# Performance work log

Measured on AMD Instinct MI355X. Metric: run time of the kernel, lower is better.

## Reference

```python
import jax, jax.numpy as jnp
import numpy as np
import math

B, N, D = 8, 2048, 64


def setup_inputs() -> dict:
    key = jax.random.key(0)
    kq, kk, kv, kd = jax.random.split(key, 4)
    Q = jax.random.normal(kq, (B, N, D), dtype=jnp.float32)
    K = jax.random.normal(kk, (B, N, D), dtype=jnp.float32)
    V = jax.random.normal(kv, (B, N, D), dtype=jnp.float32)
    dist_matrix = jax.random.uniform(kd, (N, N), dtype=jnp.float32)
    return {"Q": Q, "K": K, "V": V, "dist_matrix": dist_matrix}


def rescale_distance_matrix(dist_matrix):
    # (1 + e^1) / (1 + exp(1 - dist))
    c = 1.0
    return (c + math.e) / (c + jnp.exp(c - dist_matrix))


def reference(Q, K, V, dist_matrix):
    d_k = K.shape[-1]
    inv_sqrt_dk = 1.0 / math.sqrt(d_k)
    # [B, N, N] raw attention logits
    qk = jnp.einsum("bnd,bmd->bnm", Q, K)
    # ReLU then multiply by rescaled distance matrix [N, N] on the right
    scores = jnp.matmul(jax.nn.relu(qk), rescale_distance_matrix(dist_matrix)) * inv_sqrt_dk
    attn = jax.nn.softmax(scores, axis=-1)
    context = jnp.einsum("bnm,bmd->bnd", attn, V)
    return context
```

## Files before the change

kernel.cpp:

```cpp
#include <hip/hip_runtime.h>


typedef _Float16 f16;
typedef _Float16 f16x8 __attribute__((ext_vector_type(8)));
typedef float    f32x4 __attribute__((ext_vector_type(4)));

#define AS1C(p) ((const __attribute__((address_space(1))) void*)(p))
#define AS3(p)  ((__attribute__((address_space(3))) void*)(p))

__device__ __forceinline__ f16x8 cvt_f16x8(float4 a, float4 b){
  f16x8 v;
  v[0]=(f16)a.x; v[1]=(f16)a.y; v[2]=(f16)a.z; v[3]=(f16)a.w;
  v[4]=(f16)b.x; v[5]=(f16)b.y; v[6]=(f16)b.z; v[7]=(f16)b.w;
  return v;
}

__global__ void k_rescaleT(const float* __restrict__ Dm, f16* __restrict__ RhT){
  __shared__ f16 tl[64][65];
  const int k0 = blockIdx.x*64, m0 = blockIdx.y*64;
  const int t = threadIdx.x, c = t & 63, g = t >> 6;
#pragma unroll
  for (int i=0;i<16;++i){
    int k = g*16 + i;
    float d = Dm[(size_t)(k0 + k)*2048 + m0 + c];
    tl[k][c] = (f16)(3.7182818284590452f / (1.0f + __expf(1.0f - d)));
  }
  __syncthreads();
#pragma unroll
  for (int i=0;i<16;++i){
    int m = g*16 + i;
    RhT[(size_t)(m0 + m)*2048 + k0 + c] = tl[c][m];
  }
}

__global__ void k_vT(const float* __restrict__ V, f16* __restrict__ VhT){
  __shared__ f16 tl[64][65];
  const int b = blockIdx.y, m0 = blockIdx.x*64;
  const int t = threadIdx.x, c = t & 63, g = t >> 6;
#pragma unroll
  for (int i=0;i<16;++i){
    int m = g*16 + i;
    tl[m][c] = (f16)V[((size_t)b*2048 + m0 + m)*64 + c];
  }
  __syncthreads();
#pragma unroll
  for (int i=0;i<16;++i){
    int d = g*16 + i;
    VhT[((size_t)b*64 + d)*2048 + m0 + c] = tl[c][d];
  }
}

__launch_bounds__(256, 2)
__global__ void k_qk(const float* __restrict__ Q, const float* __restrict__ Km,
                     f16* __restrict__ Ph){
  __shared__ char shm[36864];
  f16* Qt = (f16*)shm;
  f16* Kt = (f16*)(shm + 18432);
  f16* Tt = (f16*)shm;

  const int t = threadIdx.x, w = t>>6, l = t&63, lr = l&15, q = l>>4;
  const int b = blockIdx.z, n0 = blockIdx.y*128, m0 = blockIdx.x*128;
  const int wr = (w>>1)*64, wc = (w&1)*64;
  const float* Qb = Q  + ((size_t)b*2048 + n0)*64;
  const float* Kb = Km + ((size_t)b*2048 + m0)*64;

  const int sr = t>>3, sc = t&7;
#pragma unroll
  for (int j=0;j<4;++j){
    int row = sr + 32*j;
    const float* p  = Qb + (size_t)row*64 + sc*8;
    *(f16x8*)(Qt + row*72 + sc*8) = cvt_f16x8(*(const float4*)p, *(const float4*)(p+4));
    const float* pk = Kb + (size_t)row*64 + sc*8;
    *(f16x8*)(Kt + row*72 + sc*8) = cvt_f16x8(*(const float4*)pk, *(const float4*)(pk+4));
  }
  __syncthreads();

  f32x4 acc[4][4] = {};
#pragma unroll
  for (int kc=0;kc<2;++kc){
    f16x8 af[4], bf[4];
#pragma unroll
    for (int ti=0;ti<4;++ti) af[ti] = *(const f16x8*)(Qt + (wr+16*ti+lr)*72 + kc*32 + q*8);
#pragma unroll
    for (int tj=0;tj<4;++tj) bf[tj] = *(const f16x8*)(Kt + (wc+16*tj+lr)*72 + kc*32 + q*8);
#pragma unroll
    for (int ti=0;ti<4;++ti)
#pragma unroll
      for (int tj=0;tj<4;++tj)
        acc[ti][tj] = __builtin_amdgcn_mfma_f32_16x16x32_f16(af[ti], bf[tj], acc[ti][tj], 0,0,0);
  }
  __syncthreads();
#pragma unroll
  for (int ti=0;ti<4;++ti)
#pragma unroll
    for (int tj=0;tj<4;++tj)
#pragma unroll
      for (int r=0;r<4;++r)
        Tt[(wr+16*ti+4*q+r)*136 + wc+16*tj+lr] = (f16)(fmaxf(acc[ti][tj][r],0.f)*0.125f);
  __syncthreads();
  const int g16 = t&15, r0 = t>>4;
#pragma unroll
  for (int j=0;j<8;++j){
    int row = r0 + 16*j;
    *(f16x8*)(Ph + ((size_t)b*2048 + n0 + row)*2048 + m0 + g16*8) =
        *(const f16x8*)(Tt + row*136 + g16*8);
  }
}

__launch_bounds__(256, 2)
__global__ void k_attn(const f16* __restrict__ Ph, const f16* __restrict__ RhT,
                       const f16* __restrict__ VhT, f16* __restrict__ Op,
                       float* __restrict__ mp, float* __restrict__ lp){
  __shared__ char smem[54272];
  f16*  Pbuf = (f16*)smem;
  f16*  Rbuf = (f16*)(smem + 16384);
  f16*  El   = (f16*)smem;
  float* stat_max = (float*)(smem + 49152);
  float* stat_sum = (float*)(smem + 51200);
  float* mrow = (float*)(smem + 53248);
  float* lrow = (float*)(smem + 53760);

  const int t = threadIdx.x, w = t>>6, l = t&63, lr = l&15, q = l>>4;
  const int bid = blockIdx.x;
  const int jq = bid & 3, nbb = bid >> 2, b = nbb & 7, nb = nbb >> 3;
  const int n0 = nb*128, jbase = jq*512;
  const int wc = w*64;

  const f16* Pblk = Ph  + ((size_t)b*2048 + n0)*2048;
  const f16* Vb   = VhT + (size_t)b*64*2048;

  if (t < 128){ mrow[t] = -1e30f; lrow[t] = 0.0f; }

  f32x4 Oacc[2][2][2] = {};
  const int swz = (lr>>1)&3;

  auto stage = [&](int jg, int kc){
    const int cb = kc & 1, k0 = kc*32;
#pragma unroll
    for (int i=0;i<2;++i){
      int slot = i*256 + t;
      int row = slot>>2, g = slot&3;
      int gs = (g ^ ((row>>1)&3))*8;
      __builtin_amdgcn_global_load_lds(AS1C(Pblk + (size_t)row*2048 + k0 + gs),
                                       AS3(Pbuf + cb*4096 + i*2048 + w*512), 16, 0, 0);
    }
#pragma unroll
    for (int i=0;i<4;++i){
      int slot = i*256 + t;
      int row = slot>>2, g = slot&3;
      int gs = (g ^ ((row>>1)&3))*8;
      __builtin_amdgcn_global_load_lds(AS1C(RhT + (size_t)(jg + row)*2048 + k0 + gs),
                                       AS3(Rbuf + cb*8192 + i*2048 + w*512), 16, 0, 0);
    }
  };

  stage(jbase, 0);

  for (int mt = 0; mt < 2; ++mt){
    const int jg = jbase + mt*256;
    f32x4 acc[8][4] = {};

#pragma unroll 2
    for (int kc = 0; kc < 64; ++kc){
      __syncthreads();
      if (kc < 63) stage(jg, kc+1);
      const int cb = kc & 1;
      const f16* Pb = Pbuf + cb*4096;
      const f16* Rb = Rbuf + cb*8192;
      f16x8 bf[4];
#pragma unroll
      for (int tj=0;tj<4;++tj)
        bf[tj] = *(const f16x8*)(Rb + (wc + 16*tj + lr)*32 + (q ^ swz)*8);
#pragma unroll
      for (int ti=0;ti<8;++ti){
        f16x8 af = *(const f16x8*)(Pb + (16*ti + lr)*32 + (q ^ swz)*8);
#pragma unroll
        for (int tj=0;tj<4;++tj)
          acc[ti][tj] = __builtin_amdgcn_mfma_f32_16x16x32_f16(af, bf[tj], acc[ti][tj], 0,0,0);
      }
    }

#pragma unroll
    for (int p=0;p<2;++p){
      float pm[4][4];
#pragma unroll
      for (int ti=0;ti<4;++ti)
#pragma unroll
        for (int r=0;r<4;++r)
          pm[ti][r] = fmaxf(fmaxf(acc[4*p+ti][0][r], acc[4*p+ti][1][r]),
                            fmaxf(acc[4*p+ti][2][r], acc[4*p+ti][3][r]));
#pragma unroll
      for (int mm=1;mm<16;mm<<=1)
#pragma unroll
        for (int ti=0;ti<4;++ti)
#pragma unroll
          for (int r=0;r<4;++r)
            pm[ti][r] = fmaxf(pm[ti][r], __shfl_xor(pm[ti][r], mm));
      if (lr == 0)
#pragma unroll
        for (int ti=0;ti<4;++ti)
#pragma unroll
          for (int r=0;r<4;++r)
            stat_max[(64*p + 16*ti + 4*q + r)*4 + w] = pm[ti][r];
      __syncthreads();

      float Mn[4][4], ps[4][4], al[2][4];
#pragma unroll
      for (int ti=0;ti<4;++ti)
#pragma unroll
        for (int r=0;r<4;++r){
          int row = 64*p + 16*ti + 4*q + r;
          float4 s4 = *(const float4*)&stat_max[row*4];
          float tm = fmaxf(fmaxf(s4.x,s4.y), fmaxf(s4.z,s4.w));
          float mo = mrow[row];
          float M  = fmaxf(mo, tm);
          Mn[ti][r] = M;
          ps[ti][r] = 0.f;
          if ((ti>>1) == (w&1)) al[ti&1][r] = __expf(mo - M);
        }
#pragma unroll
      for (int ti=0;ti<4;++ti)
#pragma unroll
        for (int tj=0;tj<4;++tj)
#pragma unroll
          for (int r=0;r<4;++r){
            float e = __expf(acc[4*p+ti][tj][r] - Mn[ti][r]);
            ps[ti][r] += e;
            El[(16*ti + 4*q + r)*264 + wc + 16*tj + lr] = (f16)e;
          }
#pragma unroll
      for (int mm=1;mm<16;mm<<=1)
#pragma unroll
        for (int ti=0;ti<4;++ti)
#pragma unroll
          for (int r=0;r<4;++r)
            ps[ti][r] += __shfl_xor(ps[ti][r], mm);
      if (lr == 0)
#pragma unroll
        for (int ti=0;ti<4;++ti)
#pragma unroll
          for (int r=0;r<4;++r)
            stat_sum[(64*p + 16*ti + 4*q + r)*4 + w] = ps[ti][r];
#pragma unroll
      for (int a=0;a<2;++a)
#pragma unroll
        for (int bb=0;bb<2;++bb)
#pragma unroll
          for (int r=0;r<4;++r)
            Oacc[p][a][bb][r] *= al[a][r];
      __syncthreads();

      if (t < 64){
        int row = 64*p + t;
        float m_o = mrow[row], tm = -1e30f, s4 = 0.f;
#pragma unroll
        for (int i=0;i<4;++i){ tm = fmaxf(tm, stat_max[row*4+i]); s4 += stat_sum[row*4+i]; }
        float M = fmaxf(m_o, tm);
        lrow[row] = lrow[row]*__expf(m_o - M) + s4;
        mrow[row] = M;
      }

      const int erb = 32*(w&1), vcb = 32*(w>>1);
#pragma unroll
      for (int ks=0; ks<8; ++ks){
        f16x8 ae[2], bv[2];
#pragma unroll
        for (int a=0;a<2;++a)
          ae[a] = *(const f16x8*)(El + (erb + 16*a + lr)*264 + ks*32 + q*8);
#pragma unroll
        for (int bb=0;bb<2;++bb)
          bv[bb] = *(const f16x8*)(Vb + (size_t)(vcb + 16*bb + lr)*2048 + jg + ks*32 + q*8);
#pragma unroll
        for (int a=0;a<2;++a)
#pragma unroll
          for (int bb=0;bb<2;++bb)
            Oacc[p][a][bb] = __builtin_amdgcn_mfma_f32_16x16x32_f16(ae[a], bv[bb], Oacc[p][a][bb], 0,0,0);
      }
      __syncthreads();
    }

    if (mt == 0) stage(jbase + 256, 0);
  }

  __syncthreads();
#pragma unroll
  for (int p=0;p<2;++p)
#pragma unroll
    for (int a=0;a<2;++a)
#pragma unroll
      for (int bb=0;bb<2;++bb)
#pragma unroll
        for (int r=0;r<4;++r){
          int row = 64*p + 32*(w&1) + 16*a + 4*q + r;
          int col = 32*(w>>1) + 16*bb + lr;
          Op[((size_t)bid*128 + row)*64 + col] = (f16)Oacc[p][a][bb][r];
        }
  if (t < 128){ mp[bid*128 + t] = mrow[t]; lp[bid*128 + t] = lrow[t]; }
}

__global__ void k_comb(const f16* __restrict__ Op, const float* __restrict__ mp,
                       const float* __restrict__ lp, float* __restrict__ out){
  const int rb = blockIdx.x;
  const int b = rb & 7, nb = rb >> 3;
  const int bid0 = rb*4;
  const int t = threadIdx.x;
  const int row = t >> 1, half = t & 1;

  float m_[4], a_[4];
  float M = -1e30f, den = 0.f;
#pragma unroll
  for (int i=0;i<4;++i){ m_[i] = mp[(bid0+i)*128 + row]; M = fmaxf(M, m_[i]); }
#pragma unroll
  for (int i=0;i<4;++i){ a_[i] = __expf(m_[i] - M); den += a_[i]*lp[(bid0+i)*128 + row]; }
  float inv = 1.0f / den;

#pragma unroll
  for (int g=0;g<4;++g){
    int c0 = half*32 + g*8;
    float o[8] = {};
#pragma unroll
    for (int i=0;i<4;++i){
      f16x8 v = *(const f16x8*)(Op + ((size_t)(bid0+i)*128 + row)*64 + c0);
#pragma unroll
      for (int e=0;e<8;++e) o[e] += a_[i]*(float)v[e];
    }
    float4 o0, o1;
    o0.x=o[0]*inv; o0.y=o[1]*inv; o0.z=o[2]*inv; o0.w=o[3]*inv;
    o1.x=o[4]*inv; o1.y=o[5]*inv; o1.z=o[6]*inv; o1.w=o[7]*inv;
    float* dst = out + ((size_t)b*2048 + nb*128 + row)*64 + c0;
    *(float4*)dst = o0;
    *(float4*)(dst+4) = o1;
  }
}

extern "C" void kernel_launch(void* const* d_in, const int* in_sizes, int n_in,
                              void* d_out, int out_size, void* d_ws, size_t ws_size,
                              hipStream_t stream){
  (void)in_sizes; (void)n_in; (void)out_size; (void)ws_size;
  const float* Q  = (const float*)d_in[0];
  const float* K  = (const float*)d_in[1];
  const float* V  = (const float*)d_in[2];
  const float* Dm = (const float*)d_in[3];
  float* out = (float*)d_out;
  char* ws = (char*)d_ws;
  f16* Ph  = (f16*)ws;
  f16* RhT = (f16*)(ws + (size_t)64*1024*1024);
  f16* VhT = (f16*)(ws + (size_t)72*1024*1024);
  f16* Op  = (f16*)(ws + (size_t)74*1024*1024);
  float* mpp = (float*)(ws + (size_t)74*1024*1024 + (size_t)512*128*64*2);
  float* lpp = mpp + 512*128;

  k_rescaleT<<<dim3(32,32), 256, 0, stream>>>(Dm, RhT);
  k_vT      <<<dim3(32,8),  256, 0, stream>>>(V, VhT);
  k_qk      <<<dim3(16,16,8), 256, 0, stream>>>(Q, K, Ph);
  k_attn    <<<dim3(512),   256, 0, stream>>>(Ph, RhT, VhT, Op, mpp, lpp);
  k_comb    <<<dim3(128),   256, 0, stream>>>(Op, mpp, lpp, out);
}
```

Before: 260.1 us.

## Fuse QK^T+ReLU into attention kernel, recomputing P tiles on the fly

New measurement: 272.3 us. 1.05x slower.

```diff
diff --git a/kernel.cpp b/kernel.cpp
--- a/kernel.cpp
+++ b/kernel.cpp
@@ -50,239 +50,226 @@
   }
 }
 
+__global__ void k_cvtK(const float* __restrict__ K, f16* __restrict__ Kh){
+  size_t i = ((size_t)blockIdx.x*256 + threadIdx.x)*8;
+  *(f16x8*)(Kh + i) = cvt_f16x8(*(const float4*)(K+i), *(const float4*)(K+i+4));
+}
+
 __launch_bounds__(256, 2)
-__global__ void k_qk(const float* __restrict__ Q, const float* __restrict__ Km,
-                     f16* __restrict__ Ph){
-  __shared__ char shm[36864];
-  f16* Qt = (f16*)shm;
-  f16* Kt = (f16*)(shm + 18432);
-  f16* Tt = (f16*)shm;
-
-  const int t = threadIdx.x, w = t>>6, l = t&63, lr = l&15, q = l>>4;
-  const int b = blockIdx.z, n0 = blockIdx.y*128, m0 = blockIdx.x*128;
-  const int wr = (w>>1)*64, wc = (w&1)*64;
-  const float* Qb = Q  + ((size_t)b*2048 + n0)*64;
-  const float* Kb = Km + ((size_t)b*2048 + m0)*64;
-
-  const int sr = t>>3, sc = t&7;
-#pragma unroll
-  for (int j=0;j<4;++j){
-    int row = sr + 32*j;
-    const float* p  = Qb + (size_t)row*64 + sc*8;
-    *(f16x8*)(Qt + row*72 + sc*8) = cvt_f16x8(*(const float4*)p, *(const float4*)(p+4));
-    const float* pk = Kb + (size_t)row*64 + sc*8;
-    *(f16x8*)(Kt + row*72 + sc*8) = cvt_f16x8(*(const float4*)pk, *(const float4*)(pk+4));
-  }
-  __syncthreads();
-
-  f32x4 acc[4][4] = {};
-#pragma unroll
-  for (int kc=0;kc<2;++kc){
-    f16x8 af[4], bf[4];
-#pragma unroll
-    for (int ti=0;ti<4;++ti) af[ti] = *(const f16x8*)(Qt + (wr+16*ti+lr)*72 + kc*32 + q*8);
-#pragma unroll
-    for (int tj=0;tj<4;++tj) bf[tj] = *(const f16x8*)(Kt + (wc+16*tj+lr)*72 + kc*32 + q*8);
-#pragma unroll
-    for (int ti=0;ti<4;++ti)
-#pragma unroll
-      for (int tj=0;tj<4;++tj)
-        acc[ti][tj] = __builtin_amdgcn_mfma_f32_16x16x32_f16(af[ti], bf[tj], acc[ti][tj], 0,0,0);
-  }
-  __syncthreads();
-#pragma unroll
-  for (int ti=0;ti<4;++ti)
-#pragma unroll
-    for (int tj=0;tj<4;++tj)
-#pragma unroll
-      for (int r=0;r<4;++r)
-        Tt[(wr+16*ti+4*q+r)*136 + wc+16*tj+lr] = (f16)(fmaxf(acc[ti][tj][r],0.f)*0.125f);
-  __syncthreads();
-  const int g16 = t&15, r0 = t>>4;
-#pragma unroll
-  for (int j=0;j<8;++j){
-    int row = r0 + 16*j;
-    *(f16x8*)(Ph + ((size_t)b*2048 + n0 + row)*2048 + m0 + g16*8) =
-        *(const f16x8*)(Tt + row*136 + g16*8);
-  }
-}
-
-__launch_bounds__(256, 2)
-__global__ void k_attn(const f16* __restrict__ Ph, const f16* __restrict__ RhT,
-                       const f16* __restrict__ VhT, f16* __restrict__ Op,
-                       float* __restrict__ mp, float* __restrict__ lp){
-  __shared__ char smem[54272];
+__global__ void k_attn(const float* __restrict__ Q, const f16* __restrict__ Kh,
+                       const f16* __restrict__ RhT, const f16* __restrict__ VhT,
+                       f16* __restrict__ Op, float* __restrict__ mp,
+                       float* __restrict__ lp){
+  __shared__ char smem[62464];
   f16*  Pbuf = (f16*)smem;
-  f16*  Rbuf = (f16*)(smem + 16384);
+  f16*  Kbuf = (f16*)(smem + 16384);
+  f16*  Rbuf = (f16*)(smem + 24576);
   f16*  El   = (f16*)smem;
-  float* stat_max = (float*)(smem + 49152);
-  float* stat_sum = (float*)(smem + 51200);
-  float* mrow = (float*)(smem + 53248);
-  float* lrow = (float*)(smem + 53760);
+  float* stat_max = (float*)(smem + 57344);
+  float* stat_sum = (float*)(smem + 59392);
+  float* mrow = (float*)(smem + 61440);
+  float* lrow = (float*)(smem + 61952);
 
   const int t = threadIdx.x, w = t>>6, l = t&63, lr = l&15, q = l>>4;
   const int bid = blockIdx.x;
-  const int jq = bid & 3, nbb = bid >> 2, b = nbb & 7, nb = nbb >> 3;
-  const int n0 = nb*128, jbase = jq*512;
+  const int jq = bid & 7, nbb = bid >> 3, b = nbb & 7, nb = nbb >> 3;
+  const int n0 = nb*128, jg = jq*256;
   const int wc = w*64;
 
-  const f16* Pblk = Ph  + ((size_t)b*2048 + n0)*2048;
-  const f16* Vb   = VhT + (size_t)b*64*2048;
+  const float* Qb = Q   + ((size_t)b*2048 + n0)*64;
+  const f16*  Khb = Kh  + (size_t)b*2048*64;
+  const f16*  Vb  = VhT + (size_t)b*64*2048;
 
   if (t < 128){ mrow[t] = -1e30f; lrow[t] = 0.0f; }
 
+  f16x8 qf[2][2];
+#pragma unroll
+  for (int a=0;a<2;++a)
+#pragma unroll
+    for (int dc=0;dc<2;++dc){
+      const float* p = Qb + (size_t)(32*w + 16*a + lr)*64 + dc*32 + q*8;
+      qf[a][dc] = cvt_f16x8(*(const float4*)p, *(const float4*)(p+4));
+    }
+
   f32x4 Oacc[2][2][2] = {};
-  const int swz = (lr>>1)&3;
-
-  auto stage = [&](int jg, int kc){
+  const int swz  = (lr>>1)&3;
+  const int kswz = lr&7;
+
+  auto stageK = [&](int kc){
+    const int cb = kc & 1;
+    int row = t>>3, g = t&7;
+    int gs = (g ^ (row&7))*8;
+    __builtin_amdgcn_global_load_lds(AS1C(Khb + (size_t)(kc*32 + row)*64 + gs),
+                                     AS3(Kbuf + cb*2048 + w*512), 16, 0, 0);
+  };
+  auto stageR = [&](int kc){
     const int cb = kc & 1, k0 = kc*32;
 #pragma unroll
-    for (int i=0;i<2;++i){
-      int slot = i*256 + t;
-      int row = slot>>2, g = slot&3;
-      int gs = (g ^ ((row>>1)&3))*8;
-      __builtin_amdgcn_global_load_lds(AS1C(Pblk + (size_t)row*2048 + k0 + gs),
-                                       AS3(Pbuf + cb*4096 + i*2048 + w*512), 16, 0, 0);
-    }
-#pragma unroll
     for (int i=0;i<4;++i){
-      int slot = i*256 + t;
-      int row = slot>>2, g = slot&3;
+      int slot = i*256 + t, row = slot>>2, g = slot&3;
       int gs = (g ^ ((row>>1)&3))*8;
       __builtin_amdgcn_global_load_lds(AS1C(RhT + (size_t)(jg + row)*2048 + k0 + gs),
                                        AS3(Rbuf + cb*8192 + i*2048 + w*512), 16, 0, 0);
     }
   };
-
-  stage(jbase, 0);
-
-  for (int mt = 0; mt < 2; ++mt){
-    const int jg = jbase + mt*256;
-    f32x4 acc[8][4] = {};
-
+  auto computeP = [&](int kc){
+    const int cb = kc & 1;
+    const f16* Kb = Kbuf + cb*2048;
+    f16x8 bf[2][2];
+#pragma unroll
+    for (int bb=0;bb<2;++bb)
+#pragma unroll
+      for (int dc=0;dc<2;++dc)
+        bf[bb][dc] = *(const f16x8*)(Kb + (16*bb + lr)*64 + ((dc*4 + q) ^ kswz)*8);
+    f32x4 pa[2][2] = {};
+#pragma unroll
+    for (int dc=0;dc<2;++dc)
+#pragma unroll
+      for (int a=0;a<2;++a)
+#pragma unroll
+        for (int bb=0;bb<2;++bb)
+          pa[a][bb] = __builtin_amdgcn_mfma_f32_16x16x32_f16(qf[a][dc], bf[bb][dc], pa[a][bb], 0,0,0);
+    f16* Pw = Pbuf + cb*4096;
+#pragma unroll
+    for (int a=0;a<2;++a)
+#pragma unroll
+      for (int bb=0;bb<2;++bb)
+#pragma unroll
+        for (int r=0;r<4;++r){
+          int row = 32*w + 16*a + 4*q + r;
+          int m   = 16*bb + lr;
+          Pw[row*32 + ((m>>3) ^ ((row>>1)&3))*8 + (m&7)] =
+              (f16)(fmaxf(pa[a][bb][r], 0.f)*0.125f);
+        }
+  };
+
+  stageK(0);
+  __syncthreads();
+  stageR(0); stageK(1);
+  computeP(0);
+
+  f32x4 acc[8][4] = {};
 #pragma unroll 2
-    for (int kc = 0; kc < 64; ++kc){
-      __syncthreads();
-      if (kc < 63) stage(jg, kc+1);
-      const int cb = kc & 1;
-      const f16* Pb = Pbuf + cb*4096;
-      const f16* Rb = Rbuf + cb*8192;
-      f16x8 bf[4];
+  for (int kc = 0; kc < 64; ++kc){
+    __syncthreads();
+    if (kc < 63) stageR(kc+1);
+    if (kc < 62) stageK(kc+2);
+    if (kc < 63) computeP(kc+1);
+    const int cb = kc & 1;
+    const f16* Pb = Pbuf + cb*4096;
+    const f16* Rb = Rbuf + cb*8192;
+    f16x8 bf2[4];
+#pragma unroll
+    for (int tj=0;tj<4;++tj)
+      bf2[tj] = *(const f16x8*)(Rb + (wc + 16*tj + lr)*32 + (q ^ swz)*8);
+#pragma unroll
+    for (int ti=0;ti<8;++ti){
+      f16x8 af = *(const f16x8*)(Pb + (16*ti + lr)*32 + (q ^ swz)*8);
 #pragma unroll
       for (int tj=0;tj<4;++tj)
-        bf[tj] = *(const f16x8*)(Rb + (wc + 16*tj + lr)*32 + (q ^ swz)*8);
-#pragma unroll
-      for (int ti=0;ti<8;++ti){
-        f16x8 af = *(const f16x8*)(Pb + (16*ti + lr)*32 + (q ^ swz)*8);
-#pragma unroll
-        for (int tj=0;tj<4;++tj)
-          acc[ti][tj] = __builtin_amdgcn_mfma_f32_16x16x32_f16(af, bf[tj], acc[ti][tj], 0,0,0);
+        acc[ti][tj] = __builtin_amdgcn_mfma_f32_16x16x32_f16(af, bf2[tj], acc[ti][tj], 0,0,0);
+    }
+  }
+
+#pragma unroll
+  for (int p=0;p<2;++p){
+    float pm[4][4];
+#pragma unroll
+    for (int ti=0;ti<4;++ti)
+#pragma unroll
+      for (int r=0;r<4;++r)
+        pm[ti][r] = fmaxf(fmaxf(acc[4*p+ti][0][r], acc[4*p+ti][1][r]),
+                          fmaxf(acc[4*p+ti][2][r], acc[4*p+ti][3][r]));
+#pragma unroll
+    for (int mm=1;mm<16;mm<<=1)
+#pragma unroll
+      for (int ti=0;ti<4;++ti)
+#pragma unroll
+        for (int r=0;r<4;++r)
+          pm[ti][r] = fmaxf(pm[ti][r], __shfl_xor(pm[ti][r], mm));
+    if (lr == 0)
+#pragma unroll
+      for (int ti=0;ti<4;++ti)
+#pragma unroll
+        for (int r=0;r<4;++r)
+          stat_max[(64*p + 16*ti + 4*q + r)*4 + w] = pm[ti][r];
+    __syncthreads();
+
+    float Mn[4][4], ps[4][4], al[2][4];
+#pragma unroll
+    for (int ti=0;ti<4;++ti)
+#pragma unroll
+      for (int r=0;r<4;++r){
+        int row = 64*p + 16*ti + 4*q + r;
+        float4 s4 = *(const float4*)&stat_max[row*4];
+        float tm = fmaxf(fmaxf(s4.x,s4.y), fmaxf(s4.z,s4.w));
+        float mo = mrow[row];
+        float M  = fmaxf(mo, tm);
+        Mn[ti][r] = M;
+        ps[ti][r] = 0.f;
+        if ((ti>>1) == (w&1)) al[ti&1][r] = __expf(mo - M);
       }
-    }
-
-#pragma unroll
-    for (int p=0;p<2;++p){
-      float pm[4][4];
+#pragma unroll
+    for (int ti=0;ti<4;++ti)
+#pragma unroll
+      for (int tj=0;tj<4;++tj)
+#pragma unroll
+        for (int r=0;r<4;++r){
+          float e = __expf(acc[4*p+ti][tj][r] - Mn[ti][r]);
+          ps[ti][r] += e;
+          El[(16*ti + 4*q + r)*264 + wc + 16*tj + lr] = (f16)e;
+        }
+#pragma unroll
+    for (int mm=1;mm<16;mm<<=1)
 #pragma unroll
       for (int ti=0;ti<4;++ti)
 #pragma unroll
         for (int r=0;r<4;++r)
-          pm[ti][r] = fmaxf(fmaxf(acc[4*p+ti][0][r], acc[4*p+ti][1][r]),
-                            fmaxf(acc[4*p+ti][2][r], acc[4*p+ti][3][r]));
-#pragma unroll
-      for (int mm=1;mm<16;mm<<=1)
-#pragma unroll
-        for (int ti=0;ti<4;++ti)
-#pragma unroll
-          for (int r=0;r<4;++r)
-            pm[ti][r] = fmaxf(pm[ti][r], __shfl_xor(pm[ti][r], mm));
-      if (lr == 0)
-#pragma unroll
-        for (int ti=0;ti<4;++ti)
-#pragma unroll
-          for (int r=0;r<4;++r)
-            stat_max[(64*p + 16*ti + 4*q + r)*4 + w] = pm[ti][r];
-      __syncthreads();
-
-      float Mn[4][4], ps[4][4], al[2][4];
+          ps[ti][r] += __shfl_xor(ps[ti][r], mm);
+    if (lr == 0)
 #pragma unroll
       for (int ti=0;ti<4;++ti)
 #pragma unroll
-        for (int r=0;r<4;++r){
-          int row = 64*p + 16*ti + 4*q + r;
-          float4 s4 = *(const float4*)&stat_max[row*4];
-          float tm = fmaxf(fmaxf(s4.x,s4.y), fmaxf(s4.z,s4.w));
-          float mo = mrow[row];
-          float M  = fmaxf(mo, tm);
-          Mn[ti][r] = M;
-          ps[ti][r] = 0.f;
-          if ((ti>>1) == (w&1)) al[ti&1][r] = __expf(mo - M);
-        }
-#pragma unroll
-      for (int ti=0;ti<4;++ti)
-#pragma unroll
-        for (int tj=0;tj<4;++tj)
-#pragma unroll
-          for (int r=0;r<4;++r){
-            float e = __expf(acc[4*p+ti][tj][r] - Mn[ti][r]);
-            ps[ti][r] += e;
-            El[(16*ti + 4*q + r)*264 + wc + 16*tj + lr] = (f16)e;
-          }
-#pragma unroll
-      for (int mm=1;mm<16;mm<<=1)
-#pragma unroll
-        for (int ti=0;ti<4;++ti)
-#pragma unroll
-          for (int r=0;r<4;++r)
-            ps[ti][r] += __shfl_xor(ps[ti][r], mm);
-      if (lr == 0)
-#pragma unroll
-        for (int ti=0;ti<4;++ti)
-#pragma unroll
-          for (int r=0;r<4;++r)
-            stat_sum[(64*p + 16*ti + 4*q + r)*4 + w] = ps[ti][r];
+        for (int r=0;r<4;++r)
+          stat_sum[(64*p + 16*ti + 4*q + r)*4 + w] = ps[ti][r];
+#pragma unroll
+    for (int a=0;a<2;++a)
+#pragma unroll
+      for (int bb=0;bb<2;++bb)
+#pragma unroll
+        for (int r=0;r<4;++r)
+          Oacc[p][a][bb][r] *= al[a][r];
+    __syncthreads();
+
+    if (t < 64){
+      int row = 64*p + t;
+      float m_o = mrow[row], tm = -1e30f, s4 = 0.f;
+#pragma unroll
+      for (int i=0;i<4;++i){ tm = fmaxf(tm, stat_max[row*4+i]); s4 += stat_sum[row*4+i]; }
+      float M = fmaxf(m_o, tm);
+      lrow[row] = lrow[row]*__expf(m_o - M) + s4;
+      mrow[row] = M;
+    }
+
+    const int erb = 32*(w&1), vcb = 32*(w>>1);
+#pragma unroll
+    for (int ks=0; ks<8; ++ks){
+      f16x8 ae[2], bv[2];
 #pragma unroll
       for (int a=0;a<2;++a)
+        ae[a] = *(const f16x8*)(El + (erb + 16*a + lr)*264 + ks*32 + q*8);
+#pragma unroll
+      for (int bb=0;bb<2;++bb)
+        bv[bb] = *(const f16x8*)(Vb + (size_t)(vcb + 16*bb + lr)*2048 + jg + ks*32 + q*8);
+#pragma unroll
+      for (int a=0;a<2;++a)
 #pragma unroll
         for (int bb=0;bb<2;++bb)
-#pragma unroll
-          for (int r=0;r<4;++r)
-            Oacc[p][a][bb][r] *= al[a][r];
-      __syncthreads();
-
-      if (t < 64){
-        int row = 64*p + t;
-        float m_o = mrow[row], tm = -1e30f, s4 = 0.f;
-#pragma unroll
-        for (int i=0;i<4;++i){ tm = fmaxf(tm, stat_max[row*4+i]); s4 += stat_sum[row*4+i]; }
-        float M = fmaxf(m_o, tm);
-        lrow[row] = lrow[row]*__expf(m_o - M) + s4;
-        mrow[row] = M;
-      }
-
-      const int erb = 32*(w&1), vcb = 32*(w>>1);
-#pragma unroll
-      for (int ks=0; ks<8; ++ks){
-        f16x8 ae[2], bv[2];
-#pragma unroll
-        for (int a=0;a<2;++a)
-          ae[a] = *(const f16x8*)(El + (erb + 16*a + lr)*264 + ks*32 + q*8);
-#pragma unroll
-        for (int bb=0;bb<2;++bb)
-          bv[bb] = *(const f16x8*)(Vb + (size_t)(vcb + 16*bb + lr)*2048 + jg + ks*32 + q*8);
-#pragma unroll
-        for (int a=0;a<2;++a)
-#pragma unroll
-          for (int bb=0;bb<2;++bb)
-            Oacc[p][a][bb] = __builtin_amdgcn_mfma_f32_16x16x32_f16(ae[a], bv[bb], Oacc[p][a][bb], 0,0,0);
-      }
-      __syncthreads();
-    }
-
-    if (mt == 0) stage(jbase + 256, 0);
-  }
-
-  __syncthreads();
+          Oacc[p][a][bb] = __builtin_amdgcn_mfma_f32_16x16x32_f16(ae[a], bv[bb], Oacc[p][a][bb], 0,0,0);
+    }
+    __syncthreads();
+  }
+
 #pragma unroll
   for (int p=0;p<2;++p)
 #pragma unroll
@@ -302,16 +289,16 @@
                        const float* __restrict__ lp, float* __restrict__ out){
   const int rb = blockIdx.x;
   const int b = rb & 7, nb = rb >> 3;
-  const int bid0 = rb*4;
+  const int bid0 = rb << 3;
   const int t = threadIdx.x;
   const int row = t >> 1, half = t & 1;
 
-  float m_[4], a_[4];
+  float m_[8], a_[8];
   float M = -1e30f, den = 0.f;
 #pragma unroll
-  for (int i=0;i<4;++i){ m_[i] = mp[(bid0+i)*128 + row]; M = fmaxf(M, m_[i]); }
-#pragma unroll
-  for (int i=0;i<4;++i){ a_[i] = __expf(m_[i] - M); den += a_[i]*lp[(bid0+i)*128 + row]; }
+  for (int i=0;i<8;++i){ m_[i] = mp[(bid0+i)*128 + row]; M = fmaxf(M, m_[i]); }
+#pragma unroll
+  for (int i=0;i<8;++i){ a_[i] = __expf(m_[i] - M); den += a_[i]*lp[(bid0+i)*128 + row]; }
   float inv = 1.0f / den;
 
 #pragma unroll
@@ -319,7 +306,7 @@
     int c0 = half*32 + g*8;
     float o[8] = {};
 #pragma unroll
-    for (int i=0;i<4;++i){
+    for (int i=0;i<8;++i){
       f16x8 v = *(const f16x8*)(Op + ((size_t)(bid0+i)*128 + row)*64 + c0);
 #pragma unroll
       for (int e=0;e<8;++e) o[e] += a_[i]*(float)v[e];
@@ -343,16 +330,16 @@
   const float* Dm = (const float*)d_in[3];
   float* out = (float*)d_out;
   char* ws = (char*)d_ws;
-  f16* Ph  = (f16*)ws;
-  f16* RhT = (f16*)(ws + (size_t)64*1024*1024);
-  f16* VhT = (f16*)(ws + (size_t)72*1024*1024);
-  f16* Op  = (f16*)(ws + (size_t)74*1024*1024);
-  float* mpp = (float*)(ws + (size_t)74*1024*1024 + (size_t)512*128*64*2);
-  float* lpp = mpp + 512*128;
+  f16* RhT = (f16*)ws;
+  f16* VhT = (f16*)(ws + (size_t) 8*1024*1024);
+  f16* Kh  = (f16*)(ws + (size_t)10*1024*1024);
+  f16* Op  = (f16*)(ws + (size_t)12*1024*1024);
+  float* mpp = (float*)(ws + (size_t)28*1024*1024);
+  float* lpp = mpp + 1024*128;
 
   k_rescaleT<<<dim3(32,32), 256, 0, stream>>>(Dm, RhT);
   k_vT      <<<dim3(32,8),  256, 0, stream>>>(V, VhT);
-  k_qk      <<<dim3(16,16,8), 256, 0, stream>>>(Q, K, Ph);
-  k_attn    <<<dim3(512),   256, 0, stream>>>(Ph, RhT, VhT, Op, mpp, lpp);
+  k_cvtK    <<<dim3(512),   256, 0, stream>>>(K, Kh);
+  k_attn    <<<dim3(1024),  256, 0, stream>>>(Q, Kh, RhT, VhT, Op, mpp, lpp);
   k_comb    <<<dim3(128),   256, 0, stream>>>(Op, mpp, lpp, out);
 }
```

## Fuse preprocessing kernels into QK launch and split attention into eight column chunks

Applied to the files above, without the earlier changes.

Result: faster. 249.7 us (-4.0%).

```diff
diff --git a/kernel.cpp b/kernel.cpp
--- a/kernel.cpp
+++ b/kernel.cpp
@@ -15,51 +15,57 @@
   return v;
 }
 
-__global__ void k_rescaleT(const float* __restrict__ Dm, f16* __restrict__ RhT){
-  __shared__ f16 tl[64][65];
-  const int k0 = blockIdx.x*64, m0 = blockIdx.y*64;
-  const int t = threadIdx.x, c = t & 63, g = t >> 6;
-#pragma unroll
-  for (int i=0;i<16;++i){
-    int k = g*16 + i;
-    float d = Dm[(size_t)(k0 + k)*2048 + m0 + c];
-    tl[k][c] = (f16)(3.7182818284590452f / (1.0f + __expf(1.0f - d)));
-  }
-  __syncthreads();
-#pragma unroll
-  for (int i=0;i<16;++i){
-    int m = g*16 + i;
-    RhT[(size_t)(m0 + m)*2048 + k0 + c] = tl[c][m];
-  }
-}
-
-__global__ void k_vT(const float* __restrict__ V, f16* __restrict__ VhT){
-  __shared__ f16 tl[64][65];
-  const int b = blockIdx.y, m0 = blockIdx.x*64;
-  const int t = threadIdx.x, c = t & 63, g = t >> 6;
-#pragma unroll
-  for (int i=0;i<16;++i){
-    int m = g*16 + i;
-    tl[m][c] = (f16)V[((size_t)b*2048 + m0 + m)*64 + c];
-  }
-  __syncthreads();
-#pragma unroll
-  for (int i=0;i<16;++i){
-    int d = g*16 + i;
-    VhT[((size_t)b*64 + d)*2048 + m0 + c] = tl[c][d];
-  }
-}
-
 __launch_bounds__(256, 2)
 __global__ void k_qk(const float* __restrict__ Q, const float* __restrict__ Km,
-                     f16* __restrict__ Ph){
+                     const float* __restrict__ V, const float* __restrict__ Dm,
+                     f16* __restrict__ Ph, f16* __restrict__ RhT,
+                     f16* __restrict__ VhT){
   __shared__ char shm[36864];
+  const int bid = blockIdx.x;
+  const int t = threadIdx.x;
+
+  if (bid >= 2048){
+    f16* tl = (f16*)shm;
+    const int c = t & 63, g = t >> 6;
+    if (bid < 3072){
+      const int pid = bid - 2048;
+      const int k0 = (pid & 31)*64, m0 = (pid >> 5)*64;
+#pragma unroll
+      for (int i=0;i<16;++i){
+        int k = g*16 + i;
+        float d = Dm[(size_t)(k0 + k)*2048 + m0 + c];
+        tl[k*65 + c] = (f16)(3.7182818284590452f / (1.0f + __expf(1.0f - d)));
+      }
+      __syncthreads();
+#pragma unroll
+      for (int i=0;i<16;++i){
+        int m = g*16 + i;
+        RhT[(size_t)(m0 + m)*2048 + k0 + c] = tl[c*65 + m];
+      }
+    } else {
+      const int pid = bid - 3072;
+      const int m0 = (pid & 31)*64, b = pid >> 5;
+#pragma unroll
+      for (int i=0;i<16;++i){
+        int m = g*16 + i;
+        tl[m*65 + c] = (f16)V[((size_t)b*2048 + m0 + m)*64 + c];
+      }
+      __syncthreads();
+#pragma unroll
+      for (int i=0;i<16;++i){
+        int d = g*16 + i;
+        VhT[((size_t)b*64 + d)*2048 + m0 + c] = tl[c*65 + d];
+      }
+    }
+    return;
+  }
+
   f16* Qt = (f16*)shm;
   f16* Kt = (f16*)(shm + 18432);
   f16* Tt = (f16*)shm;
 
-  const int t = threadIdx.x, w = t>>6, l = t&63, lr = l&15, q = l>>4;
-  const int b = blockIdx.z, n0 = blockIdx.y*128, m0 = blockIdx.x*128;
+  const int w = t>>6, l = t&63, lr = l&15, q = l>>4;
+  const int m0 = (bid & 15)*128, n0 = ((bid>>4) & 15)*128, b = bid >> 8;
   const int wr = (w>>1)*64, wc = (w&1)*64;
   const float* Qb = Q  + ((size_t)b*2048 + n0)*64;
   const float* Kb = Km + ((size_t)b*2048 + m0)*64;
@@ -111,178 +117,162 @@
 __global__ void k_attn(const f16* __restrict__ Ph, const f16* __restrict__ RhT,
                        const f16* __restrict__ VhT, f16* __restrict__ Op,
                        float* __restrict__ mp, float* __restrict__ lp){
-  __shared__ char smem[54272];
+  __shared__ char smem[49152];
   f16*  Pbuf = (f16*)smem;
   f16*  Rbuf = (f16*)(smem + 16384);
   f16*  El   = (f16*)smem;
-  float* stat_max = (float*)(smem + 49152);
-  float* stat_sum = (float*)(smem + 51200);
-  float* mrow = (float*)(smem + 53248);
-  float* lrow = (float*)(smem + 53760);
+  float* stat_max = (float*)(smem + 33792);
+  float* stat_sum = (float*)(smem + 34816);
 
   const int t = threadIdx.x, w = t>>6, l = t&63, lr = l&15, q = l>>4;
   const int bid = blockIdx.x;
-  const int jq = bid & 3, nbb = bid >> 2, b = nbb & 7, nb = nbb >> 3;
-  const int n0 = nb*128, jbase = jq*512;
+  const int jq = bid & 7, nbb = bid >> 3, b = nbb & 7, nb = nbb >> 3;
+  const int n0 = nb*128, jg = jq*256;
   const int wc = w*64;
 
   const f16* Pblk = Ph  + ((size_t)b*2048 + n0)*2048;
   const f16* Vb   = VhT + (size_t)b*64*2048;
 
-  if (t < 128){ mrow[t] = -1e30f; lrow[t] = 0.0f; }
-
+  const f16* srcP[2];
+  const f16* srcR[4];
+#pragma unroll
+  for (int i=0;i<2;++i){
+    int slot = i*256 + t, row = slot>>2, g = slot&3;
+    srcP[i] = Pblk + (size_t)row*2048 + (g ^ ((row>>1)&3))*8;
+  }
+#pragma unroll
+  for (int i=0;i<4;++i){
+    int slot = i*256 + t, row = slot>>2, g = slot&3;
+    srcR[i] = RhT + (size_t)(jg + row)*2048 + (g ^ ((row>>1)&3))*8;
+  }
+
+  auto stage = [&](int kc){
+    const int cb = kc & 1, k0 = kc*32;
+#pragma unroll
+    for (int i=0;i<2;++i)
+      __builtin_amdgcn_global_load_lds(AS1C(srcP[i] + k0),
+                                       AS3(Pbuf + cb*4096 + i*2048 + w*512), 16, 0, 0);
+#pragma unroll
+    for (int i=0;i<4;++i)
+      __builtin_amdgcn_global_load_lds(AS1C(srcR[i] + k0),
+                                       AS3(Rbuf + cb*8192 + i*2048 + w*512), 16, 0, 0);
+  };
+
+  const int swz = (lr>>1)&3;
+  f32x4 acc[8][4] = {};
   f32x4 Oacc[2][2][2] = {};
-  const int swz = (lr>>1)&3;
-
-  auto stage = [&](int jg, int kc){
-    const int cb = kc & 1, k0 = kc*32;
-#pragma unroll
-    for (int i=0;i<2;++i){
-      int slot = i*256 + t;
-      int row = slot>>2, g = slot&3;
-      int gs = (g ^ ((row>>1)&3))*8;
-      __builtin_amdgcn_global_load_lds(AS1C(Pblk + (size_t)row*2048 + k0 + gs),
-                                       AS3(Pbuf + cb*4096 + i*2048 + w*512), 16, 0, 0);
+
+  stage(0);
+#pragma unroll 2
+  for (int kc = 0; kc < 64; ++kc){
+    __syncthreads();
+    if (kc < 63) stage(kc+1);
+    const int cb = kc & 1;
+    const f16* Pb = Pbuf + cb*4096;
+    const f16* Rb = Rbuf + cb*8192;
+    f16x8 bf[4];
+#pragma unroll
+    for (int tj=0;tj<4;++tj)
+      bf[tj] = *(const f16x8*)(Rb + (wc + 16*tj + lr)*32 + (q ^ swz)*8);
+#pragma unroll
+    for (int ti=0;ti<8;++ti){
+      f16x8 af = *(const f16x8*)(Pb + (16*ti + lr)*32 + (q ^ swz)*8);
+#pragma unroll
+      for (int tj=0;tj<4;++tj)
+        acc[ti][tj] = __builtin_amdgcn_mfma_f32_16x16x32_f16(af, bf[tj], acc[ti][tj], 0,0,0);
     }
-#pragma unroll
-    for (int i=0;i<4;++i){
-      int slot = i*256 + t;
-      int row = slot>>2, g = slot&3;
-      int gs = (g ^ ((row>>1)&3))*8;
-      __builtin_amdgcn_global_load_lds(AS1C(RhT + (size_t)(jg + row)*2048 + k0 + gs),
-                                       AS3(Rbuf + cb*8192 + i*2048 + w*512), 16, 0, 0);
+  }
+  __syncthreads();
+
+#pragma unroll
+  for (int p=0;p<2;++p){
+    float pm[4][4];
+#pragma unroll
+    for (int ti=0;ti<4;++ti)
+#pragma unroll
+      for (int r=0;r<4;++r)
+        pm[ti][r] = fmaxf(fmaxf(acc[4*p+ti][0][r], acc[4*p+ti][1][r]),
+                          fmaxf(acc[4*p+ti][2][r], acc[4*p+ti][3][r]));
+#pragma unroll
+    for (int mm=1;mm<16;mm<<=1)
+#pragma unroll
+      for (int ti=0;ti<4;++ti)
+#pragma unroll
+        for (int r=0;r<4;++r)
+          pm[ti][r] = fmaxf(pm[ti][r], __shfl_xor(pm[ti][r], mm));
+    if (lr == 0)
+#pragma unroll
+      for (int ti=0;ti<4;++ti)
+#pragma unroll
+        for (int r=0;r<4;++r)
+          stat_max[(16*ti + 4*q + r)*4 + w] = pm[ti][r];
+    __syncthreads();
+
+    float Mn[4][4], ps[4][4];
+#pragma unroll
+    for (int ti=0;ti<4;++ti)
+#pragma unroll
+      for (int r=0;r<4;++r){
+        int row = 16*ti + 4*q + r;
+        float4 s4 = *(const float4*)&stat_max[row*4];
+        Mn[ti][r] = fmaxf(fmaxf(s4.x,s4.y), fmaxf(s4.z,s4.w));
+        ps[ti][r] = 0.f;
+      }
+#pragma unroll
+    for (int ti=0;ti<4;++ti)
+#pragma unroll
+      for (int tj=0;tj<4;++tj)
+#pragma unroll
+        for (int r=0;r<4;++r){
+          float e = __expf(acc[4*p+ti][tj][r] - Mn[ti][r]);
+          ps[ti][r] += e;
+          El[(16*ti + 4*q + r)*264 + wc + 16*tj + lr] = (f16)e;
+        }
+#pragma unroll
+    for (int mm=1;mm<16;mm<<=1)
+#pragma unroll
+      for (int ti=0;ti<4;++ti)
+#pragma unroll
+        for (int r=0;r<4;++r)
+          ps[ti][r] += __shfl_xor(ps[ti][r], mm);
+    if (lr == 0)
+#pragma unroll
+      for (int ti=0;ti<4;++ti)
+#pragma unroll
+        for (int r=0;r<4;++r)
+          stat_sum[(16*ti + 4*q + r)*4 + w] = ps[ti][r];
+    __syncthreads();
+
+    if (w == 0 && lr == 0)
+#pragma unroll
+      for (int ti=0;ti<4;++ti)
+#pragma unroll
+        for (int r=0;r<4;++r){
+          int row = 16*ti + 4*q + r;
+          float4 s4 = *(const float4*)&stat_sum[row*4];
+          mp[bid*128 + 64*p + row] = Mn[ti][r];
+          lp[bid*128 + 64*p + row] = s4.x + s4.y + s4.z + s4.w;
+        }
+
+    const int erb = 32*(w&1), vcb = 32*(w>>1);
+#pragma unroll
+    for (int ks=0; ks<8; ++ks){
+      f16x8 ae[2], bv[2];
+#pragma unroll
+      for (int a=0;a<2;++a)
+        ae[a] = *(const f16x8*)(El + (erb + 16*a + lr)*264 + ks*32 + q*8);
+#pragma unroll
+      for (int bb=0;bb<2;++bb)
+        bv[bb] = *(const f16x8*)(Vb + (size_t)(vcb + 16*bb + lr)*2048 + jg + ks*32 + q*8);
+#pragma unroll
+      for (int a=0;a<2;++a)
+#pragma unroll
+        for (int bb=0;bb<2;++bb)
+          Oacc[p][a][bb] = __builtin_amdgcn_mfma_f32_16x16x32_f16(ae[a], bv[bb], Oacc[p][a][bb], 0,0,0);
     }
-  };
-
-  stage(jbase, 0);
-
-  for (int mt = 0; mt < 2; ++mt){
-    const int jg = jbase + mt*256;
-    f32x4 acc[8][4] = {};
-
-#pragma unroll 2
-    for (int kc = 0; kc < 64; ++kc){
-      __syncthreads();
-      if (kc < 63) stage(jg, kc+1);
-      const int cb = kc & 1;
-      const f16* Pb = Pbuf + cb*4096;
-      const f16* Rb = Rbuf + cb*8192;
-      f16x8 bf[4];
-#pragma unroll
-      for (int tj=0;tj<4;++tj)
-        bf[tj] = *(const f16x8*)(Rb + (wc + 16*tj + lr)*32 + (q ^ swz)*8);
-#pragma unroll
-      for (int ti=0;ti<8;++ti){
-        f16x8 af = *(const f16x8*)(Pb + (16*ti + lr)*32 + (q ^ swz)*8);
-#pragma unroll
-        for (int tj=0;tj<4;++tj)
-          acc[ti][tj] = __builtin_amdgcn_mfma_f32_16x16x32_f16(af, bf[tj], acc[ti][tj], 0,0,0);
-      }
-    }
-
-#pragma unroll
-    for (int p=0;p<2;++p){
-      float pm[4][4];
-#pragma unroll
-      for (int ti=0;ti<4;++ti)
-#pragma unroll
-        for (int r=0;r<4;++r)
-          pm[ti][r] = fmaxf(fmaxf(acc[4*p+ti][0][r], acc[4*p+ti][1][r]),
-                            fmaxf(acc[4*p+ti][2][r], acc[4*p+ti][3][r]));
-#pragma unroll
-      for (int mm=1;mm<16;mm<<=1)
-#pragma unroll
-        for (int ti=0;ti<4;++ti)
-#pragma unroll
-          for (int r=0;r<4;++r)
-            pm[ti][r] = fmaxf(pm[ti][r], __shfl_xor(pm[ti][r], mm));
-      if (lr == 0)
-#pragma unroll
-        for (int ti=0;ti<4;++ti)
-#pragma unroll
-          for (int r=0;r<4;++r)
-            stat_max[(64*p + 16*ti + 4*q + r)*4 + w] = pm[ti][r];
-      __syncthreads();
-
-      float Mn[4][4], ps[4][4], al[2][4];
-#pragma unroll
-      for (int ti=0;ti<4;++ti)
-#pragma unroll
-        for (int r=0;r<4;++r){
-          int row = 64*p + 16*ti + 4*q + r;
-          float4 s4 = *(const float4*)&stat_max[row*4];
-          float tm = fmaxf(fmaxf(s4.x,s4.y), fmaxf(s4.z,s4.w));
-          float mo = mrow[row];
-          float M  = fmaxf(mo, tm);
-          Mn[ti][r] = M;
-          ps[ti][r] = 0.f;
-          if ((ti>>1) == (w&1)) al[ti&1][r] = __expf(mo - M);
-        }
-#pragma unroll
-      for (int ti=0;ti<4;++ti)
-#pragma unroll
-        for (int tj=0;tj<4;++tj)
-#pragma unroll
-          for (int r=0;r<4;++r){
-            float e = __expf(acc[4*p+ti][tj][r] - Mn[ti][r]);
-            ps[ti][r] += e;
-            El[(16*ti + 4*q + r)*264 + wc + 16*tj + lr] = (f16)e;
-          }
-#pragma unroll
-      for (int mm=1;mm<16;mm<<=1)
-#pragma unroll
-        for (int ti=0;ti<4;++ti)
-#pragma unroll
-          for (int r=0;r<4;++r)
-            ps[ti][r] += __shfl_xor(ps[ti][r], mm);
-      if (lr == 0)
-#pragma unroll
-        for (int ti=0;ti<4;++ti)
-#pragma unroll
-          for (int r=0;r<4;++r)
-            stat_sum[(64*p + 16*ti + 4*q + r)*4 + w] = ps[ti][r];
-#pragma unroll
-      for (int a=0;a<2;++a)
-#pragma unroll
-        for (int bb=0;bb<2;++bb)
-#pragma unroll
-          for (int r=0;r<4;++r)
-            Oacc[p][a][bb][r] *= al[a][r];
-      __syncthreads();
-
-      if (t < 64){
-        int row = 64*p + t;
-        float m_o = mrow[row], tm = -1e30f, s4 = 0.f;
-#pragma unroll
-        for (int i=0;i<4;++i){ tm = fmaxf(tm, stat_max[row*4+i]); s4 += stat_sum[row*4+i]; }
-        float M = fmaxf(m_o, tm);
-        lrow[row] = lrow[row]*__expf(m_o - M) + s4;
-        mrow[row] = M;
-      }
-
-      const int erb = 32*(w&1), vcb = 32*(w>>1);
-#pragma unroll
-      for (int ks=0; ks<8; ++ks){
-        f16x8 ae[2], bv[2];
-#pragma unroll
-        for (int a=0;a<2;++a)
-          ae[a] = *(const f16x8*)(El + (erb + 16*a + lr)*264 + ks*32 + q*8);
-#pragma unroll
-        for (int bb=0;bb<2;++bb)
-          bv[bb] = *(const f16x8*)(Vb + (size_t)(vcb + 16*bb + lr)*2048 + jg + ks*32 + q*8);
-#pragma unroll
-        for (int a=0;a<2;++a)
-#pragma unroll
-          for (int bb=0;bb<2;++bb)
-            Oacc[p][a][bb] = __builtin_amdgcn_mfma_f32_16x16x32_f16(ae[a], bv[bb], Oacc[p][a][bb], 0,0,0);
-      }
-      __syncthreads();
-    }
-
-    if (mt == 0) stage(jbase + 256, 0);
-  }
-
-  __syncthreads();
+    __syncthreads();
+  }
+
 #pragma unroll
   for (int p=0;p<2;++p)
 #pragma unroll
@@ -295,23 +285,22 @@
           int col = 32*(w>>1) + 16*bb + lr;
           Op[((size_t)bid*128 + row)*64 + col] = (f16)Oacc[p][a][bb][r];
         }
-  if (t < 128){ mp[bid*128 + t] = mrow[t]; lp[bid*128 + t] = lrow[t]; }
 }
 
 __global__ void k_comb(const f16* __restrict__ Op, const float* __restrict__ mp,
                        const float* __restrict__ lp, float* __restrict__ out){
   const int rb = blockIdx.x;
   const int b = rb & 7, nb = rb >> 3;
-  const int bid0 = rb*4;
+  const int bid0 = rb << 3;
   const int t = threadIdx.x;
   const int row = t >> 1, half = t & 1;
 
-  float m_[4], a_[4];
+  float m_[8], a_[8];
   float M = -1e30f, den = 0.f;
 #pragma unroll
-  for (int i=0;i<4;++i){ m_[i] = mp[(bid0+i)*128 + row]; M = fmaxf(M, m_[i]); }
-#pragma unroll
-  for (int i=0;i<4;++i){ a_[i] = __expf(m_[i] - M); den += a_[i]*lp[(bid0+i)*128 + row]; }
+  for (int i=0;i<8;++i){ m_[i] = mp[(bid0+i)*128 + row]; M = fmaxf(M, m_[i]); }
+#pragma unroll
+  for (int i=0;i<8;++i){ a_[i] = __expf(m_[i] - M); den += a_[i]*lp[(bid0+i)*128 + row]; }
   float inv = 1.0f / den;
 
 #pragma unroll
@@ -319,7 +308,7 @@
     int c0 = half*32 + g*8;
     float o[8] = {};
 #pragma unroll
-    for (int i=0;i<4;++i){
+    for (int i=0;i<8;++i){
       f16x8 v = *(const f16x8*)(Op + ((size_t)(bid0+i)*128 + row)*64 + c0);
 #pragma unroll
       for (int e=0;e<8;++e) o[e] += a_[i]*(float)v[e];
@@ -347,12 +336,10 @@
   f16* RhT = (f16*)(ws + (size_t)64*1024*1024);
   f16* VhT = (f16*)(ws + (size_t)72*1024*1024);
   f16* Op  = (f16*)(ws + (size_t)74*1024*1024);
-  float* mpp = (float*)(ws + (size_t)74*1024*1024 + (size_t)512*128*64*2);
-  float* lpp = mpp + 512*128;
-
-  k_rescaleT<<<dim3(32,32), 256, 0, stream>>>(Dm, RhT);
-  k_vT      <<<dim3(32,8),  256, 0, stream>>>(V, VhT);
-  k_qk      <<<dim3(16,16,8), 256, 0, stream>>>(Q, K, Ph);
-  k_attn    <<<dim3(512),   256, 0, stream>>>(Ph, RhT, VhT, Op, mpp, lpp);
-  k_comb    <<<dim3(128),   256, 0, stream>>>(Op, mpp, lpp, out);
-}
+  float* mpp = (float*)(ws + (size_t)90*1024*1024);
+  float* lpp = mpp + 1024*128;
+
+  k_qk   <<<dim3(3328), 256, 0, stream>>>(Q, K, V, Dm, Ph, RhT, VhT);
+  k_attn <<<dim3(1024), 256, 0, stream>>>(Ph, RhT, VhT, Op, mpp, lpp);
+  k_comb <<<dim3(128),  256, 0, stream>>>(Op, mpp, lpp, out);
+}
```
